# Kernel tuning notes

Hardware: AMD Instinct MI355X
Metric: run time of the kernel (lower is better)

## Reference

```python
import jax, jax.numpy as jnp
import numpy as np
from jax import lax

N, CIN, P, CH, COUT = 1024, 3, 14, 256, 3
DN = ('NCHW', 'OIHW', 'NCHW')


def _conv(x, w, b, pad=1):
    y = lax.conv_general_dilated(x, w, (1, 1), [(pad, pad), (pad, pad)], dimension_numbers=DN)
    return y + b[None, :, None, None]


def _conv_transpose(x, w_t, b):
    # PyTorch ConvTranspose2d(k=3, stride=2, padding=1, output_padding=1):
    # equivalent to conv with lhs_dilation=2, padding (k-1-p, k-1-p+op) = (1, 2),
    # kernel with in/out swapped and spatially flipped. w_t: [in, out, 3, 3]
    w = jnp.flip(jnp.transpose(w_t, (1, 0, 2, 3)), axis=(2, 3))  # [out, in, 3, 3]
    y = lax.conv_general_dilated(x, w, (1, 1), [(1, 2), (1, 2)], lhs_dilation=(2, 2),
                                 dimension_numbers=DN)
    return y + b[None, :, None, None]


def setup_inputs() -> dict:
    key = jax.random.key(0)
    ks = jax.random.split(key, 16)
    s3 = lambda cin: 1.0 / np.sqrt(cin * 9)
    inp = {"x": jax.random.normal(ks[0], (N, CIN, P, P), dtype=jnp.float32)}
    inp["w1"] = jax.random.normal(ks[1], (CH, CIN, 3, 3), jnp.float32) * s3(CIN)
    inp["b1"] = jnp.zeros((CH,), jnp.float32)
    inp["w2"] = jax.random.normal(ks[2], (CH, CH, 3, 3), jnp.float32) * s3(CH)
    inp["b2"] = jnp.zeros((CH,), jnp.float32)
    inp["w3"] = jax.random.normal(ks[3], (CH, CH, 3, 3), jnp.float32) * s3(CH)
    inp["b3"] = jnp.zeros((CH,), jnp.float32)
    inp["w4"] = jax.random.normal(ks[4], (CH, CH, 3, 3), jnp.float32) * s3(CH)
    inp["b4"] = jnp.zeros((CH,), jnp.float32)
    inp["wt"] = jax.random.normal(ks[5], (CH, CH, 3, 3), jnp.float32) * s3(CH)  # [in, out, kh, kw]
    inp["bt"] = jnp.zeros((CH,), jnp.float32)
    inp["w5"] = jax.random.normal(ks[6], (COUT, CH, 1, 1), jnp.float32) * (1.0 / np.sqrt(CH))
    inp["b5"] = jnp.zeros((COUT,), jnp.float32)
    return inp


def reference(x, w1, b1, w2, b2, w3, b3, w4, b4, wt, bt, w5, b5):
    h = jax.nn.relu(_conv(x, w1, b1))
    h = jax.nn.relu(_conv(h, w2, b2))
    h = jax.nn.relu(_conv(h, w3, b3))
    h = jax.nn.relu(_conv(h, w4, b4))
    h = jax.nn.relu(_conv_transpose(h, wt, bt))  # [N, 256, 2P, 2P]
    h = _conv(h, w5, b5, pad=0)                   # 1x1 conv -> [N, 3, 2P, 2P]
    return jax.nn.sigmoid(h)
```

## Files before the change

### kernel.cpp

```cpp
#include <hip/hip_runtime.h>
#include <hip/hip_fp16.h>

typedef _Float16 half8 __attribute__((ext_vector_type(8)));
typedef _Float16 half4 __attribute__((ext_vector_type(4)));
typedef float floatx4 __attribute__((ext_vector_type(4)));

#define PLANE 65536
#define PK_ELEMS 589824

__global__ void repack_kernel(const float* __restrict__ w2, const float* __restrict__ w3,
                              const float* __restrict__ w4, const float* __restrict__ wt,
                              _Float16* __restrict__ pk) {
    int t = blockIdx.x * 256 + threadIdx.x;
    int l = t & 63;
    int idx = t >> 6;
    int nt = idx & 15; idx >>= 4;
    int ks = idx & 7;  idx >>= 3;
    int tap = idx % 9;
    int layer = idx / 9;
    int co = nt * 16 + (l & 15);
    int ci0 = ks * 32 + (l >> 4) * 8;
    const float* w = (layer == 0) ? w2 : (layer == 1) ? w3 : (layer == 2) ? w4 : wt;
    _Float16* dst = pk + (size_t)layer * PK_ELEMS + (((size_t)(tap * 8 + ks) * 16 + nt) * 64 + l) * 8;
    if (layer < 3) {
        for (int j = 0; j < 8; ++j)
            dst[j] = (_Float16)w[(co * 256 + (ci0 + j)) * 9 + tap];
    } else {
        int ky = tap / 3, kx = tap % 3;
        for (int j = 0; j < 8; ++j)
            dst[j] = (_Float16)w[((ci0 + j) * 256 + co) * 9 + (2 - ky) * 3 + (2 - kx)];
    }
}

__global__ __launch_bounds__(1024, 4) void conv1_kernel(const float* __restrict__ x,
                                                        const float* __restrict__ w1,
                                                        const float* __restrict__ b1,
                                                        _Float16* __restrict__ act) {
    __shared__ float inl[3][16][16];
    __shared__ float lw[256 * 27];
    __shared__ float lb1[256];
    int n = blockIdx.x, tid = threadIdx.x;
    if (tid < 768) ((float*)inl)[tid] = 0.f;
    __syncthreads();
    for (int i = tid; i < 3 * 196; i += 1024) {
        int ci = i / 196, r = i % 196, y = r / 14, xx = r % 14;
        inl[ci][y + 1][xx + 1] = x[(size_t)n * 588 + i];
    }
    for (int i = tid; i < 256 * 27; i += 1024) lw[i] = w1[i];
    if (tid < 256) lb1[tid] = b1[tid];
    __syncthreads();
    int p = tid >> 2, q = tid & 3;
    int py = p >> 4, px = p & 15;
    _Float16* ga = act + (size_t)n * PLANE + p * 256;
    int sw = (p & 7) << 3;
    if (py == 0 || py == 15 || px == 0 || px == 15) {
        for (int ci = 0; ci < 64; ++ci) { int co = q + ci * 4; ga[co ^ sw] = (_Float16)0.f; }
    } else {
        float vin[27];
        #pragma unroll
        for (int ci = 0; ci < 3; ++ci)
            #pragma unroll
            for (int ky = 0; ky < 3; ++ky)
                #pragma unroll
                for (int kx = 0; kx < 3; ++kx)
                    vin[ci * 9 + ky * 3 + kx] = inl[ci][py - 1 + ky][px - 1 + kx];
        for (int ci = 0; ci < 64; ++ci) {
            int co = q + ci * 4;
            float acc = lb1[co];
            const float* wp = &lw[co * 27];
            #pragma unroll
            for (int k = 0; k < 27; ++k) acc += vin[k] * wp[k];
            ga[co ^ sw] = (_Float16)fmaxf(acc, 0.f);
        }
    }
}


#define INIT_ACC(BIASPTR)                                                        \
    {                                                                            \
        _Pragma("unroll")                                                        \
        for (int ni = 0; ni < 4; ++ni) {                                         \
            floatx4 bv;                                                          \
            _Pragma("unroll")                                                    \
            for (int reg = 0; reg < 4; ++reg)                                    \
                bv[reg] = (BIASPTR)[(cg * 4 + ni) * 16 + kg * 4 + reg];          \
            _Pragma("unroll")                                                    \
            for (int i = 0; i < 7; ++i) acc[i][ni] = bv;                         \
        }                                                                        \
    }

#define ACCUM_TAP(PKT, DOFF)                                                     \
    {                                                                            \
        const _Float16* pkt_ = (PKT);                                            \
        const _Float16* bpx_[7];                                                 \
        int swj_[7];                                                             \
        _Pragma("unroll")                                                        \
        for (int j = 0; j < 7; ++j) {                                            \
            int ipx = pp[j] + (DOFF);                                            \
            bpx_[j] = plane + ipx * 256;                                         \
            swj_[j] = (ipx & 7) << 3;                                            \
        }                                                                        \
        half8 a_[4], an_[4], bb_[7];                                             \
        _Pragma("unroll")                                                        \
        for (int ni = 0; ni < 4; ++ni)                                           \
            a_[ni] = *(const half8*)(pkt_ + ((cg * 4 + ni) * 64 + lane) * 8);    \
        _Pragma("clang loop unroll(disable)")                                    \
        for (int ks = 0; ks < 8; ++ks) {                                         \
            int kk = (ks * 4 + kg) << 3;                                         \
            _Pragma("unroll")                                                    \
            for (int j = 0; j < 7; ++j)                                          \
                bb_[j] = *(const half8*)(bpx_[j] + (kk ^ swj_[j]));              \
            if (ks < 7) {                                                        \
                _Pragma("unroll")                                                \
                for (int ni = 0; ni < 4; ++ni)                                   \
                    an_[ni] = *(const half8*)(pkt_ + (((ks + 1) * 16 + cg * 4 + ni) * 64 + lane) * 8); \
            }                                                                    \
            _Pragma("unroll")                                                    \
            for (int j = 0; j < 7; ++j) {                                        \
                acc[j][0] = __builtin_amdgcn_mfma_f32_16x16x32_f16(a_[0], bb_[j], acc[j][0], 0, 0, 0); \
                acc[j][1] = __builtin_amdgcn_mfma_f32_16x16x32_f16(a_[1], bb_[j], acc[j][1], 0, 0, 0); \
                acc[j][2] = __builtin_amdgcn_mfma_f32_16x16x32_f16(a_[2], bb_[j], acc[j][2], 0, 0, 0); \
                acc[j][3] = __builtin_amdgcn_mfma_f32_16x16x32_f16(a_[3], bb_[j], acc[j][3], 0, 0, 0); \
            }                                                                    \
            if (ks < 7) {                                                        \
                _Pragma("unroll")                                                \
                for (int ni = 0; ni < 4; ++ni) a_[ni] = an_[ni];                 \
            }                                                                    \
        }                                                                        \
    }

#define EPILOGUE(RY, RX)                                                         \
    {                                                                            \
        _Pragma("unroll")                                                        \
        for (int i = 0; i < 7; ++i) {                                            \
            float s0 = 0.f, s1 = 0.f, s2 = 0.f;                                  \
            _Pragma("unroll")                                                    \
            for (int ni = 0; ni < 4; ++ni) {                                     \
                int co0 = (cg * 4 + ni) * 16 + kg * 4;                           \
                _Pragma("unroll")                                                \
                for (int reg = 0; reg < 4; ++reg) {                              \
                    float v = fmaxf(acc[i][ni][reg], 0.f);                       \
                    s0 += v * w5l[co0 + reg];                                    \
                    s1 += v * w5l[256 + co0 + reg];                              \
                    s2 += v * w5l[512 + co0 + reg];                              \
                }                                                                \
            }                                                                    \
            s0 += __shfl_xor(s0, 16, 64); s0 += __shfl_xor(s0, 32, 64);          \
            s1 += __shfl_xor(s1, 16, 64); s1 += __shfl_xor(s1, 32, 64);          \
            s2 += __shfl_xor(s2, 16, 64); s2 += __shfl_xor(s2, 32, 64);          \
            if (lane < 14) {                                                     \
                int pt_ = pg + 2 * i;                                            \
                int pix = (2 * pt_ + (RY)) * 28 + 2 * lane + (RX);               \
                atomicAdd(&o3[pix * 3 + 0], s0);                                 \
                atomicAdd(&o3[pix * 3 + 1], s1);                                 \
                atomicAdd(&o3[pix * 3 + 2], s2);                                 \
            }                                                                    \
        }                                                                        \
    }

__global__ __launch_bounds__(512, 2) void fused_kernel(const _Float16* __restrict__ act,
                                                       const _Float16* __restrict__ pk,
                                                       const float* __restrict__ b2,
                                                       const float* __restrict__ b3,
                                                       const float* __restrict__ b4,
                                                       const float* __restrict__ bt,
                                                       const float* __restrict__ w5,
                                                       const float* __restrict__ b5,
                                                       float* __restrict__ out) {
    __shared__ _Float16 plane[PLANE];
    __shared__ float o3[2352];
    __shared__ float w5l[768];
    int n = blockIdx.x, tid = threadIdx.x;
    const _Float16* ga = act + (size_t)n * PLANE;
    #pragma unroll
    for (int i = 0; i < 16; ++i)
        *(uint4*)(plane + (i * 512 + tid) * 8) = *(const uint4*)(ga + (i * 512 + tid) * 8);
    for (int i = tid; i < 2352; i += 512) o3[i] = b5[i % 3];
    for (int i = tid; i < 768; i += 512) w5l[i] = w5[i];

    int lane = tid & 63, wid = tid >> 6;
    int cg = wid >> 1, pg = wid & 1;
    int col = lane & 15, kg = lane >> 4;

    int pp[7];
    {
        int xc = (col < 14) ? col : 13;
        #pragma unroll
        for (int i = 0; i < 7; ++i) pp[i] = (pg + 2 * i + 1) * 16 + xc + 1;
    }
    bool colok = (col < 14);
    __syncthreads();

    floatx4 acc[7][4];

    for (int L = 0; L < 3; ++L) {
        const _Float16* pkL = pk + (size_t)L * PK_ELEMS;
        const float* bias = (L == 0) ? b2 : (L == 1) ? b3 : b4;
        INIT_ACC(bias)
        for (int tap = 0; tap < 9; ++tap) {
            int doff = (tap / 3) * 16 + (tap % 3) - 17;
            ACCUM_TAP(pkL + (size_t)tap * 65536, doff)
        }
        __syncthreads();
        #pragma unroll
        for (int i = 0; i < 7; ++i) {
            int ppix = pp[i];
            int sw = (ppix & 7) << 3;
            if (colok) {
                #pragma unroll
                for (int ni = 0; ni < 4; ++ni) {
                    int co0 = (cg * 4 + ni) * 16 + kg * 4;
                    half4 h;
                    #pragma unroll
                    for (int reg = 0; reg < 4; ++reg) h[reg] = (_Float16)fmaxf(acc[i][ni][reg], 0.f);
                    *(half4*)(plane + ppix * 256 + (co0 ^ sw)) = h;
                }
            }
        }
        __syncthreads();
    }

    const _Float16* pkT = pk + (size_t)3 * PK_ELEMS;
    INIT_ACC(bt)
    ACCUM_TAP(pkT + 4 * 65536, 0)
    EPILOGUE(0, 0)
    INIT_ACC(bt)
    ACCUM_TAP(pkT + 3 * 65536, 0)
    ACCUM_TAP(pkT + 5 * 65536, 1)
    EPILOGUE(0, 1)
    INIT_ACC(bt)
    ACCUM_TAP(pkT + 1 * 65536, 0)
    ACCUM_TAP(pkT + 7 * 65536, 16)
    EPILOGUE(1, 0)
    INIT_ACC(bt)
    ACCUM_TAP(pkT + 0 * 65536, 0)
    ACCUM_TAP(pkT + 2 * 65536, 1)
    ACCUM_TAP(pkT + 6 * 65536, 16)
    ACCUM_TAP(pkT + 8 * 65536, 17)
    EPILOGUE(1, 1)

    __syncthreads();
    size_t ob = (size_t)n * 2352;
    for (int i = tid; i < 2352; i += 512) {
        int pix = i / 3, c = i % 3;
        float v = o3[i];
        out[ob + (size_t)c * 784 + pix] = 1.f / (1.f + __expf(-v));
    }
}

extern "C" void kernel_launch(void* const* d_in, const int* in_sizes, int n_in,
                              void* d_out, int out_size, void* d_ws, size_t ws_size,
                              hipStream_t stream) {
    const float* x  = (const float*)d_in[0];
    const float* w1 = (const float*)d_in[1];
    const float* b1 = (const float*)d_in[2];
    const float* w2 = (const float*)d_in[3];
    const float* b2 = (const float*)d_in[4];
    const float* w3 = (const float*)d_in[5];
    const float* b3 = (const float*)d_in[6];
    const float* w4 = (const float*)d_in[7];
    const float* b4 = (const float*)d_in[8];
    const float* wt = (const float*)d_in[9];
    const float* bt = (const float*)d_in[10];
    const float* w5 = (const float*)d_in[11];
    const float* b5 = (const float*)d_in[12];

    size_t need = ((size_t)1024 * PLANE + 4 * (size_t)PK_ELEMS) * sizeof(_Float16);
    if (ws_size < need) return;

    _Float16* act = (_Float16*)d_ws;
    _Float16* pk  = act + (size_t)1024 * PLANE;

    repack_kernel<<<1152, 256, 0, stream>>>(w2, w3, w4, wt, pk);
    conv1_kernel<<<1024, 1024, 0, stream>>>(x, w1, b1, act);
    fused_kernel<<<1024, 512, 0, stream>>>(act, pk, b2, b3, b4, bt, w5, b5, (float*)d_out);
}
```

Baseline: 958.6 us.

## Flatten pixel tiling to 13 tiles and use 12 waves per block

Replaces row-based 16-wide pixel tiles (14 valid columns) with a flattened 196-pixel index split into 13 full 16-pixel tiles, distributed over 3 pixel groups with 5 tiles each and the last tile only on one group. The block grows to 768 threads with 4 channel groups by 3 pixel groups. This cuts wasted MFMA work on padded columns and raises wave count per block for latency hiding, at the cost of uneven work across waves and extra index arithmetic for the div/mod pixel mapping.

New measurement: 961.6 us. Within noise of the previous version (+0.3%).

```diff
diff --git a/kernel.cpp b/kernel.cpp
--- a/kernel.cpp
+++ b/kernel.cpp
@@ -85,22 +85,17 @@
             for (int reg = 0; reg < 4; ++reg)                                    \
                 bv[reg] = (BIASPTR)[(cg * 4 + ni) * 16 + kg * 4 + reg];          \
             _Pragma("unroll")                                                    \
-            for (int i = 0; i < 7; ++i) acc[i][ni] = bv;                         \
+            for (int i = 0; i < 5; ++i) acc[i][ni] = bv;                         \
         }                                                                        \
     }
 
 #define ACCUM_TAP(PKT, DOFF)                                                     \
     {                                                                            \
         const _Float16* pkt_ = (PKT);                                            \
-        const _Float16* bpx_[7];                                                 \
-        int swj_[7];                                                             \
-        _Pragma("unroll")                                                        \
-        for (int j = 0; j < 7; ++j) {                                            \
-            int ipx = pp[j] + (DOFF);                                            \
-            bpx_[j] = plane + ipx * 256;                                         \
-            swj_[j] = (ipx & 7) << 3;                                            \
-        }                                                                        \
-        half8 a_[4], an_[4], bb_[7];                                             \
+        int poff_[5];                                                            \
+        _Pragma("unroll")                                                        \
+        for (int j = 0; j < 5; ++j) poff_[j] = (pp[j] + (DOFF)) * 256;           \
+        half8 a_[4], an_[4], bb_[5];                                             \
         _Pragma("unroll")                                                        \
         for (int ni = 0; ni < 4; ++ni)                                           \
             a_[ni] = *(const half8*)(pkt_ + ((cg * 4 + ni) * 64 + lane) * 8);    \
@@ -108,20 +103,28 @@
         for (int ks = 0; ks < 8; ++ks) {                                         \
             int kk = (ks * 4 + kg) << 3;                                         \
             _Pragma("unroll")                                                    \
-            for (int j = 0; j < 7; ++j)                                          \
-                bb_[j] = *(const half8*)(bpx_[j] + (kk ^ swj_[j]));              \
+            for (int j = 0; j < 4; ++j)                                          \
+                bb_[j] = *(const half8*)(plane + poff_[j] + (kk ^ ((poff_[j] >> 5) & 56))); \
+            if (pg == 0)                                                         \
+                bb_[4] = *(const half8*)(plane + poff_[4] + (kk ^ ((poff_[4] >> 5) & 56))); \
             if (ks < 7) {                                                        \
                 _Pragma("unroll")                                                \
                 for (int ni = 0; ni < 4; ++ni)                                   \
                     an_[ni] = *(const half8*)(pkt_ + (((ks + 1) * 16 + cg * 4 + ni) * 64 + lane) * 8); \
             }                                                                    \
             _Pragma("unroll")                                                    \
-            for (int j = 0; j < 7; ++j) {                                        \
+            for (int j = 0; j < 4; ++j) {                                        \
                 acc[j][0] = __builtin_amdgcn_mfma_f32_16x16x32_f16(a_[0], bb_[j], acc[j][0], 0, 0, 0); \
                 acc[j][1] = __builtin_amdgcn_mfma_f32_16x16x32_f16(a_[1], bb_[j], acc[j][1], 0, 0, 0); \
                 acc[j][2] = __builtin_amdgcn_mfma_f32_16x16x32_f16(a_[2], bb_[j], acc[j][2], 0, 0, 0); \
                 acc[j][3] = __builtin_amdgcn_mfma_f32_16x16x32_f16(a_[3], bb_[j], acc[j][3], 0, 0, 0); \
             }                                                                    \
+            if (pg == 0) {                                                       \
+                acc[4][0] = __builtin_amdgcn_mfma_f32_16x16x32_f16(a_[0], bb_[4], acc[4][0], 0, 0, 0); \
+                acc[4][1] = __builtin_amdgcn_mfma_f32_16x16x32_f16(a_[1], bb_[4], acc[4][1], 0, 0, 0); \
+                acc[4][2] = __builtin_amdgcn_mfma_f32_16x16x32_f16(a_[2], bb_[4], acc[4][2], 0, 0, 0); \
+                acc[4][3] = __builtin_amdgcn_mfma_f32_16x16x32_f16(a_[3], bb_[4], acc[4][3], 0, 0, 0); \
+            }                                                                    \
             if (ks < 7) {                                                        \
                 _Pragma("unroll")                                                \
                 for (int ni = 0; ni < 4; ++ni) a_[ni] = an_[ni];                 \
@@ -132,33 +135,35 @@
 #define EPILOGUE(RY, RX)                                                         \
     {                                                                            \
         _Pragma("unroll")                                                        \
-        for (int i = 0; i < 7; ++i) {                                            \
-            float s0 = 0.f, s1 = 0.f, s2 = 0.f;                                  \
-            _Pragma("unroll")                                                    \
-            for (int ni = 0; ni < 4; ++ni) {                                     \
-                int co0 = (cg * 4 + ni) * 16 + kg * 4;                           \
+        for (int i = 0; i < 5; ++i) {                                            \
+            if (i < 4 || pg == 0) {                                              \
+                float s0 = 0.f, s1 = 0.f, s2 = 0.f;                              \
                 _Pragma("unroll")                                                \
-                for (int reg = 0; reg < 4; ++reg) {                              \
-                    float v = fmaxf(acc[i][ni][reg], 0.f);                       \
-                    s0 += v * w5l[co0 + reg];                                    \
-                    s1 += v * w5l[256 + co0 + reg];                              \
-                    s2 += v * w5l[512 + co0 + reg];                              \
+                for (int ni = 0; ni < 4; ++ni) {                                 \
+                    int co0 = (cg * 4 + ni) * 16 + kg * 4;                       \
+                    _Pragma("unroll")                                            \
+                    for (int reg = 0; reg < 4; ++reg) {                          \
+                        float v = fmaxf(acc[i][ni][reg], 0.f);                   \
+                        s0 += v * w5l[co0 + reg];                                \
+                        s1 += v * w5l[256 + co0 + reg];                          \
+                        s2 += v * w5l[512 + co0 + reg];                          \
+                    }                                                            \
                 }                                                                \
-            }                                                                    \
-            s0 += __shfl_xor(s0, 16, 64); s0 += __shfl_xor(s0, 32, 64);          \
-            s1 += __shfl_xor(s1, 16, 64); s1 += __shfl_xor(s1, 32, 64);          \
-            s2 += __shfl_xor(s2, 16, 64); s2 += __shfl_xor(s2, 32, 64);          \
-            if (lane < 14) {                                                     \
-                int pt_ = pg + 2 * i;                                            \
-                int pix = (2 * pt_ + (RY)) * 28 + 2 * lane + (RX);               \
-                atomicAdd(&o3[pix * 3 + 0], s0);                                 \
-                atomicAdd(&o3[pix * 3 + 1], s1);                                 \
-                atomicAdd(&o3[pix * 3 + 2], s2);                                 \
+                s0 += __shfl_xor(s0, 16, 64); s0 += __shfl_xor(s0, 32, 64);      \
+                s1 += __shfl_xor(s1, 16, 64); s1 += __shfl_xor(s1, 32, 64);      \
+                s2 += __shfl_xor(s2, 16, 64); s2 += __shfl_xor(s2, 32, 64);      \
+                if (lane < 16 && pm[i] < 196) {                                  \
+                    int yy = pm[i] / 14, xx2 = pm[i] - yy * 14;                  \
+                    int pix = (2 * yy + (RY)) * 28 + 2 * xx2 + (RX);             \
+                    atomicAdd(&o3[pix * 3 + 0], s0);                             \
+                    atomicAdd(&o3[pix * 3 + 1], s1);                             \
+                    atomicAdd(&o3[pix * 3 + 2], s2);                             \
+                }                                                                \
             }                                                                    \
         }                                                                        \
     }
 
-__global__ __launch_bounds__(512, 2) void fused_kernel(const _Float16* __restrict__ act,
+__global__ __launch_bounds__(768, 3) void fused_kernel(const _Float16* __restrict__ act,
                                                        const _Float16* __restrict__ pk,
                                                        const float* __restrict__ b2,
                                                        const float* __restrict__ b3,
@@ -172,26 +177,27 @@
     __shared__ float w5l[768];
     int n = blockIdx.x, tid = threadIdx.x;
     const _Float16* ga = act + (size_t)n * PLANE;
+    for (int i = tid; i < 8192; i += 768)
+        *(uint4*)(plane + i * 8) = *(const uint4*)(ga + i * 8);
+    for (int i = tid; i < 2352; i += 768) o3[i] = b5[i % 3];
+    w5l[tid] = w5[tid];
+
+    int lane = tid & 63, wid = tid >> 6;
+    int cg = wid & 3, pg = wid >> 2;
+    int col = lane & 15, kg = lane >> 4;
+
+    int pp[5], pm[5];
     #pragma unroll
-    for (int i = 0; i < 16; ++i)
-        *(uint4*)(plane + (i * 512 + tid) * 8) = *(const uint4*)(ga + (i * 512 + tid) * 8);
-    for (int i = tid; i < 2352; i += 512) o3[i] = b5[i % 3];
-    for (int i = tid; i < 768; i += 512) w5l[i] = w5[i];
-
-    int lane = tid & 63, wid = tid >> 6;
-    int cg = wid >> 1, pg = wid & 1;
-    int col = lane & 15, kg = lane >> 4;
-
-    int pp[7];
-    {
-        int xc = (col < 14) ? col : 13;
-        #pragma unroll
-        for (int i = 0; i < 7; ++i) pp[i] = (pg + 2 * i + 1) * 16 + xc + 1;
-    }
-    bool colok = (col < 14);
-    __syncthreads();
-
-    floatx4 acc[7][4];
+    for (int i = 0; i < 5; ++i) {
+        int m = (pg + 3 * i) * 16 + col;
+        pm[i] = m;
+        int mc = (m < 196) ? m : 195;
+        int y = mc / 14, x = mc - y * 14;
+        pp[i] = (y + 1) * 16 + x + 1;
+    }
+    __syncthreads();
+
+    floatx4 acc[5][4];
 
     for (int L = 0; L < 3; ++L) {
         const _Float16* pkL = pk + (size_t)L * PK_ELEMS;
@@ -203,17 +209,19 @@
         }
         __syncthreads();
         #pragma unroll
-        for (int i = 0; i < 7; ++i) {
-            int ppix = pp[i];
-            int sw = (ppix & 7) << 3;
-            if (colok) {
-                #pragma unroll
-                for (int ni = 0; ni < 4; ++ni) {
-                    int co0 = (cg * 4 + ni) * 16 + kg * 4;
-                    half4 h;
+        for (int i = 0; i < 5; ++i) {
+            if (i < 4 || pg == 0) {
+                int ppix = pp[i];
+                int sw = (ppix & 7) << 3;
+                if (pm[i] < 196) {
                     #pragma unroll
-                    for (int reg = 0; reg < 4; ++reg) h[reg] = (_Float16)fmaxf(acc[i][ni][reg], 0.f);
-                    *(half4*)(plane + ppix * 256 + (co0 ^ sw)) = h;
+                    for (int ni = 0; ni < 4; ++ni) {
+                        int co0 = (cg * 4 + ni) * 16 + kg * 4;
+                        half4 h;
+                        #pragma unroll
+                        for (int reg = 0; reg < 4; ++reg) h[reg] = (_Float16)fmaxf(acc[i][ni][reg], 0.f);
+                        *(half4*)(plane + ppix * 256 + (co0 ^ sw)) = h;
+                    }
                 }
             }
         }
@@ -241,7 +249,7 @@
 
     __syncthreads();
     size_t ob = (size_t)n * 2352;
-    for (int i = tid; i < 2352; i += 512) {
+    for (int i = tid; i < 2352; i += 768) {
         int pix = i / 3, c = i % 3;
         float v = o3[i];
         out[ob + (size_t)c * 784 + pix] = 1.f / (1.f + __expf(-v));
@@ -273,5 +281,5 @@
 
     repack_kernel<<<1152, 256, 0, stream>>>(w2, w3, w4, wt, pk);
     conv1_kernel<<<1024, 1024, 0, stream>>>(x, w1, b1, act);
-    fused_kernel<<<1024, 512, 0, stream>>>(act, pk, b2, b3, b4, bt, w5, b5, (float*)d_out);
-}
+    fused_kernel<<<1024, 768, 0, stream>>>(act, pk, b2, b3, b4, bt, w5, b5, (float*)d_out);
+}
```
